# Optimization experiments

Hardware: AMD Instinct MI355X
Metric: run time of the kernel (lower is better)

The kernel has to match this reference:

```python
import jax, jax.numpy as jnp
import numpy as np

B_SZ, SEQ, D_MODEL, N_STATE = 4, 2048, 768, 16


def setup_inputs() -> dict:
    key = jax.random.key(0)
    ks = jax.random.split(key, 8)
    s = 1.0 / np.sqrt(D_MODEL)
    x = jax.random.normal(ks[0], (B_SZ, SEQ, D_MODEL), dtype=jnp.float32)
    W1 = jax.random.uniform(ks[1], (D_MODEL, D_MODEL), jnp.float32, -s, s)
    b1 = jax.random.uniform(ks[2], (D_MODEL,), jnp.float32, -s, s)
    W2 = jax.random.uniform(ks[3], (D_MODEL, N_STATE), jnp.float32, -s, s)
    b2 = jax.random.uniform(ks[4], (N_STATE,), jnp.float32, -s, s)
    W3 = jax.random.uniform(ks[5], (D_MODEL, N_STATE), jnp.float32, -s, s)
    b3 = jax.random.uniform(ks[6], (N_STATE,), jnp.float32, -s, s)
    # A: xavier_uniform over (d_model, state_size)
    a_bound = np.sqrt(6.0 / (D_MODEL + N_STATE))
    A = jax.random.uniform(ks[7], (D_MODEL, N_STATE), jnp.float32, -a_bound, a_bound)
    return {"x": x, "W1": W1, "b1": b1, "W2": W2, "b2": b2, "W3": W3, "b3": b3, "A": A}


def reference(x, W1, b1, W2, b2, W3, b3, A):
    # Input-dependent projections
    Bm = x @ W2 + b2                     # [b, l, n]
    Cm = x @ W3 + b3                     # [b, l, n]
    delta = jax.nn.softplus(x @ W1 + b1)  # [b, l, d]
    # Discretization (S6)
    dB = delta[..., None] * Bm[:, :, None, :]                 # [b, l, d, n]
    dA = jnp.exp(jnp.einsum('bld,dn->bldn', delta, A))        # [b, l, d, n]
    # Source initializes h to zeros, so the dA*h term vanishes (no recurrence).
    h0 = jnp.zeros_like(dB)
    h = dA * h0 + x[..., None] * dB                            # [b, l, d, n]
    y = jnp.einsum('bln,bldn->bld', Cm, h)                     # [b, l, d]
    return y
```

## Files before the change

### kernel.cpp

```cpp
#include <hip/hip_runtime.h>
#include <hip/hip_bf16.h>
#include <math.h>


#define M_ROWS 8192
#define DM 768
#define NS 16

typedef short bf16x8 __attribute__((ext_vector_type(8)));
typedef float f32x4 __attribute__((ext_vector_type(4)));

__device__ __forceinline__ unsigned short f2bf(float f) {
    union { float f; unsigned u; } v; v.f = f;
    unsigned r = v.u + 0x7FFF + ((v.u >> 16) & 1);
    return (unsigned short)(r >> 16);
}
__device__ __forceinline__ float bf2f(unsigned short h) {
    union { unsigned u; float f; } v; v.u = ((unsigned)h) << 16; return v.f;
}
__device__ __forceinline__ void async16(const void* g, void* l) {
    __builtin_amdgcn_global_load_lds(
        (const __attribute__((address_space(1))) void*)g,
        (__attribute__((address_space(3))) void*)l,
        16, 0, 0);
}
__device__ __forceinline__ float softplus_fast(float v) {
    return fmaxf(v, 0.f) + __logf(1.f + __expf(-fabsf(v)));
}

__global__ __launch_bounds__(256) void prep_kernel(
    const float* __restrict__ x,
    const float* __restrict__ W1,
    const float* __restrict__ W2,
    const float* __restrict__ W3,
    unsigned short* __restrict__ xb,
    unsigned short* __restrict__ w1t,
    unsigned short* __restrict__ w23t)
{
    __shared__ float tile[32][33];
    const int bid = blockIdx.x;
    const int tid = threadIdx.x;
    if (bid < 32) {
        const int n = bid, i = n >> 1;
        const float* src = (n & 1) ? W3 : W2;
        #pragma unroll
        for (int e = 0; e < 3; ++e) {
            int k = e * 256 + tid;
            w23t[n * DM + k] = f2bf(src[k * NS + i]);
        }
    } else if (bid < 608) {
        const int b2i = bid - 32;
        const int n0 = (b2i % 24) * 32, k0 = (b2i / 24) * 32;
        const int tx = tid & 31, ty = tid >> 5;
        #pragma unroll
        for (int i = 0; i < 4; ++i) {
            int k = ty + i * 8;
            tile[k][tx] = W1[(k0 + k) * DM + n0 + tx];
        }
        __syncthreads();
        #pragma unroll
        for (int i = 0; i < 4; ++i) {
            int n = ty + i * 8;
            w1t[(n0 + n) * DM + k0 + tx] = f2bf(tile[tx][n]);
        }
    } else {
        int i = (bid - 608) * 256 + tid;
        float4 v = ((const float4*)x)[i];
        ushort4 o;
        o.x = f2bf(v.x); o.y = f2bf(v.y); o.z = f2bf(v.z); o.w = f2bf(v.w);
        ((ushort4*)xb)[i] = o;
    }
}

__global__ __launch_bounds__(256) void gemm_fused_kernel(
    const unsigned short* __restrict__ xb,
    const unsigned short* __restrict__ w1t,
    const unsigned short* __restrict__ w23t,
    const float* __restrict__ b1,
    const float* __restrict__ b2, const float* __restrict__ b3,
    float* __restrict__ y)
{
    __shared__ unsigned short Al[128 * 64];
    __shared__ unsigned short Bl[64 * 64];
    __shared__ unsigned short Wl[32 * 64];
    __shared__ float spart[2][128];
    const int b = blockIdx.x;
    const int c = b & 7, j = b >> 3;
    const int m0 = (c * 8 + j / 12) * 128;
    const int n0 = (j % 12) * 64;
    const int tid  = threadIdx.x;
    const int lane = tid & 63;
    const int wave = tid >> 6;
    const int wm = wave >> 1, wn = wave & 1;
    const int l15 = lane & 15, quad = lane >> 4;

    f32x4 acc[4][2];
    f32x4 accP[4];
    #pragma unroll
    for (int i = 0; i < 4; ++i) {
        accP[i] = (f32x4){0.f, 0.f, 0.f, 0.f};
        #pragma unroll
        for (int jj = 0; jj < 2; ++jj)
            acc[i][jj] = (f32x4){0.f, 0.f, 0.f, 0.f};
    }

    for (int k0 = 0; k0 < DM; k0 += 64) {
        #pragma unroll
        for (int i = 0; i < 4; ++i) {
            int ch = tid + i * 256;
            int r = ch >> 3, jg = (ch & 7) ^ (r & 7);
            async16(xb + (m0 + r) * DM + k0 + jg * 8, Al + ch * 8);
        }
        #pragma unroll
        for (int i = 0; i < 2; ++i) {
            int ch = tid + i * 256;
            int r = ch >> 3, jg = (ch & 7) ^ (r & 7);
            async16(w1t + (n0 + r) * DM + k0 + jg * 8, Bl + ch * 8);
        }
        {
            int ch = tid;
            int r = ch >> 3, jg = (ch & 7) ^ (r & 7);
            async16(w23t + r * DM + k0 + jg * 8, Wl + ch * 8);
        }
        __syncthreads();

        #pragma unroll
        for (int kk = 0; kk < 2; ++kk) {
            bf16x8 bfr[2], wfr;
            #pragma unroll
            for (int jj = 0; jj < 2; ++jj) {
                int rb = wn * 32 + jj * 16 + l15;
                int jb = (kk * 4 + quad) ^ (rb & 7);
                bfr[jj] = *(const bf16x8*)(Bl + rb * 64 + jb * 8);
            }
            {
                int rw = wn * 16 + l15;
                int jw = (kk * 4 + quad) ^ (rw & 7);
                wfr = *(const bf16x8*)(Wl + rw * 64 + jw * 8);
            }
            #pragma unroll
            for (int i = 0; i < 4; ++i) {
                int rr = wm * 64 + i * 16 + l15;
                int ja = (kk * 4 + quad) ^ (rr & 7);
                bf16x8 af = *(const bf16x8*)(Al + rr * 64 + ja * 8);
                #pragma unroll
                for (int jj = 0; jj < 2; ++jj)
                    acc[i][jj] = __builtin_amdgcn_mfma_f32_16x16x32_bf16(
                        af, bfr[jj], acc[i][jj], 0, 0, 0);
                accP[i] = __builtin_amdgcn_mfma_f32_16x16x32_bf16(
                    af, wfr, accP[i], 0, 0, 0);
            }
        }
        __syncthreads();
    }

    {
        const int p = wn * 8 + (l15 >> 1);
        const float bB = b2[p], bC = b3[p];
        #pragma unroll
        for (int i = 0; i < 4; ++i) {
            float sacc[4];
            #pragma unroll
            for (int r = 0; r < 4; ++r) {
                float v = accP[i][r];
                float pv = __shfl_xor(v, 1, 64);
                sacc[r] = (l15 & 1) ? (pv + bB) * (v + bC)
                                    : (v + bB) * (pv + bC);
                sacc[r] += __shfl_xor(sacc[r], 1, 64);
                sacc[r] += __shfl_xor(sacc[r], 2, 64);
                sacc[r] += __shfl_xor(sacc[r], 4, 64);
                sacc[r] += __shfl_xor(sacc[r], 8, 64);
            }
            if (l15 == 0) {
                #pragma unroll
                for (int r = 0; r < 4; ++r)
                    spart[wn][wm * 64 + i * 16 + quad * 4 + r] = 0.5f * sacc[r];
            }
        }
    }
    __syncthreads();

    #pragma unroll
    for (int i = 0; i < 4; ++i) {
        const int rl = wm * 64 + i * 16 + quad * 4;
        const int rowbase = m0 + rl;
        float sv4[4];
        #pragma unroll
        for (int r = 0; r < 4; ++r)
            sv4[r] = spart[0][rl + r] + spart[1][rl + r];
        #pragma unroll
        for (int jj = 0; jj < 2; ++jj) {
            int gcol = n0 + wn * 32 + jj * 16 + l15;
            float bias = b1[gcol];
            #pragma unroll
            for (int r = 0; r < 4; ++r) {
                int grow = rowbase + r;
                float v = acc[i][jj][r] + bias;
                float sp = softplus_fast(v);
                float xv = bf2f(xb[grow * DM + gcol]);
                y[grow * DM + gcol] = xv * sp * sv4[r];
            }
        }
    }
}

extern "C" void kernel_launch(void* const* d_in, const int* in_sizes, int n_in,
                              void* d_out, int out_size, void* d_ws, size_t ws_size,
                              hipStream_t stream) {
    const float* x  = (const float*)d_in[0];
    const float* W1 = (const float*)d_in[1];
    const float* b1 = (const float*)d_in[2];
    const float* W2 = (const float*)d_in[3];
    const float* b2 = (const float*)d_in[4];
    const float* W3 = (const float*)d_in[5];
    const float* b3 = (const float*)d_in[6];
    float* y = (float*)d_out;

    unsigned short* xb   = (unsigned short*)d_ws;
    unsigned short* w1t  = (unsigned short*)((char*)d_ws + 12582912);
    unsigned short* w23t = (unsigned short*)((char*)d_ws + 13762560);

    prep_kernel<<<6752, 256, 0, stream>>>(x, W1, W2, W3, xb, w1t, w23t);
    gemm_fused_kernel<<<768, 256, 0, stream>>>(xb, w1t, w23t, b1, b2, b3, y);
}
```

Measured before the change: 112.1 us.

## Fuse x bf16 conversion into GEMM A-tile load, drop xb staging buffer

```diff
diff --git a/kernel.cpp b/kernel.cpp
--- a/kernel.cpp
+++ b/kernel.cpp
@@ -8,6 +8,7 @@
 #define NS 16
 
 typedef short bf16x8 __attribute__((ext_vector_type(8)));
+typedef unsigned short u16x8 __attribute__((ext_vector_type(8)));
 typedef float f32x4 __attribute__((ext_vector_type(4)));
 
 __device__ __forceinline__ unsigned short f2bf(float f) {
@@ -15,8 +16,9 @@
     unsigned r = v.u + 0x7FFF + ((v.u >> 16) & 1);
     return (unsigned short)(r >> 16);
 }
-__device__ __forceinline__ float bf2f(unsigned short h) {
-    union { unsigned u; float f; } v; v.u = ((unsigned)h) << 16; return v.f;
+__device__ __forceinline__ unsigned short cvtbf(float f) {
+    __hip_bfloat16 h = __float2bfloat16(f);
+    return *reinterpret_cast<unsigned short*>(&h);
 }
 __device__ __forceinline__ void async16(const void* g, void* l) {
     __builtin_amdgcn_global_load_lds(
@@ -29,11 +31,9 @@
 }
 
 __global__ __launch_bounds__(256) void prep_kernel(
-    const float* __restrict__ x,
     const float* __restrict__ W1,
     const float* __restrict__ W2,
     const float* __restrict__ W3,
-    unsigned short* __restrict__ xb,
     unsigned short* __restrict__ w1t,
     unsigned short* __restrict__ w23t)
 {
@@ -48,7 +48,7 @@
             int k = e * 256 + tid;
             w23t[n * DM + k] = f2bf(src[k * NS + i]);
         }
-    } else if (bid < 608) {
+    } else {
         const int b2i = bid - 32;
         const int n0 = (b2i % 24) * 32, k0 = (b2i / 24) * 32;
         const int tx = tid & 31, ty = tid >> 5;
@@ -63,17 +63,11 @@
             int n = ty + i * 8;
             w1t[(n0 + n) * DM + k0 + tx] = f2bf(tile[tx][n]);
         }
-    } else {
-        int i = (bid - 608) * 256 + tid;
-        float4 v = ((const float4*)x)[i];
-        ushort4 o;
-        o.x = f2bf(v.x); o.y = f2bf(v.y); o.z = f2bf(v.z); o.w = f2bf(v.w);
-        ((ushort4*)xb)[i] = o;
     }
 }
 
 __global__ __launch_bounds__(256) void gemm_fused_kernel(
-    const unsigned short* __restrict__ xb,
+    const float* __restrict__ x,
     const unsigned short* __restrict__ w1t,
     const unsigned short* __restrict__ w23t,
     const float* __restrict__ b1,
@@ -105,11 +99,14 @@
     }
 
     for (int k0 = 0; k0 < DM; k0 += 64) {
+        float4 va[8];
         #pragma unroll
         for (int i = 0; i < 4; ++i) {
             int ch = tid + i * 256;
             int r = ch >> 3, jg = (ch & 7) ^ (r & 7);
-            async16(xb + (m0 + r) * DM + k0 + jg * 8, Al + ch * 8);
+            const float4* src = (const float4*)(x + (m0 + r) * DM + k0 + jg * 8);
+            va[2 * i]     = src[0];
+            va[2 * i + 1] = src[1];
         }
         #pragma unroll
         for (int i = 0; i < 2; ++i) {
@@ -121,6 +118,17 @@
             int ch = tid;
             int r = ch >> 3, jg = (ch & 7) ^ (r & 7);
             async16(w23t + r * DM + k0 + jg * 8, Wl + ch * 8);
+        }
+        #pragma unroll
+        for (int i = 0; i < 4; ++i) {
+            int ch = tid + i * 256;
+            float4 a = va[2 * i], bb = va[2 * i + 1];
+            u16x8 o;
+            o[0] = cvtbf(a.x);  o[1] = cvtbf(a.y);
+            o[2] = cvtbf(a.z);  o[3] = cvtbf(a.w);
+            o[4] = cvtbf(bb.x); o[5] = cvtbf(bb.y);
+            o[6] = cvtbf(bb.z); o[7] = cvtbf(bb.w);
+            *(u16x8*)(Al + ch * 8) = o;
         }
         __syncthreads();
 
@@ -197,7 +205,7 @@
                 int grow = rowbase + r;
                 float v = acc[i][jj][r] + bias;
                 float sp = softplus_fast(v);
-                float xv = bf2f(xb[grow * DM + gcol]);
+                float xv = x[grow * DM + gcol];
                 y[grow * DM + gcol] = xv * sp * sv4[r];
             }
         }
@@ -216,10 +224,9 @@
     const float* b3 = (const float*)d_in[6];
     float* y = (float*)d_out;
 
-    unsigned short* xb   = (unsigned short*)d_ws;
-    unsigned short* w1t  = (unsigned short*)((char*)d_ws + 12582912);
-    unsigned short* w23t = (unsigned short*)((char*)d_ws + 13762560);
-
-    prep_kernel<<<6752, 256, 0, stream>>>(x, W1, W2, W3, xb, w1t, w23t);
-    gemm_fused_kernel<<<768, 256, 0, stream>>>(xb, w1t, w23t, b1, b2, b3, y);
-}
+    unsigned short* w1t  = (unsigned short*)d_ws;
+    unsigned short* w23t = (unsigned short*)((char*)d_ws + 1179648);
+
+    prep_kernel<<<608, 256, 0, stream>>>(W1, W2, W3, w1t, w23t);
+    gemm_fused_kernel<<<768, 256, 0, stream>>>(x, w1t, w23t, b1, b2, b3, y);
+}
```

After: 115.7 us. 3.3% more time.

## Double-buffer GEMM LDS tiles and load W2/W3 fragments directly to registers

Applied to the files above, without the earlier changes.

```diff
diff --git a/kernel.cpp b/kernel.cpp
--- a/kernel.cpp
+++ b/kernel.cpp
@@ -6,6 +6,7 @@
 #define M_ROWS 8192
 #define DM 768
 #define NS 16
+#define NT 12
 
 typedef short bf16x8 __attribute__((ext_vector_type(8)));
 typedef float f32x4 __attribute__((ext_vector_type(4)));
@@ -27,6 +28,8 @@
 __device__ __forceinline__ float softplus_fast(float v) {
     return fmaxf(v, 0.f) + __logf(1.f + __expf(-fabsf(v)));
 }
+
+#define FENCE() __builtin_amdgcn_sched_barrier(0)
 
 __global__ __launch_bounds__(256) void prep_kernel(
     const float* __restrict__ x,
@@ -80,9 +83,8 @@
     const float* __restrict__ b2, const float* __restrict__ b3,
     float* __restrict__ y)
 {
-    __shared__ unsigned short Al[128 * 64];
-    __shared__ unsigned short Bl[64 * 64];
-    __shared__ unsigned short Wl[32 * 64];
+    __shared__ unsigned short Al[2][128 * 64];
+    __shared__ unsigned short Bl[2][64 * 64];
     __shared__ float spart[2][128];
     const int b = blockIdx.x;
     const int c = b & 7, j = b >> 3;
@@ -104,45 +106,62 @@
             acc[i][jj] = (f32x4){0.f, 0.f, 0.f, 0.f};
     }
 
-    for (int k0 = 0; k0 < DM; k0 += 64) {
-        #pragma unroll
-        for (int i = 0; i < 4; ++i) {
-            int ch = tid + i * 256;
-            int r = ch >> 3, jg = (ch & 7) ^ (r & 7);
-            async16(xb + (m0 + r) * DM + k0 + jg * 8, Al + ch * 8);
-        }
-        #pragma unroll
-        for (int i = 0; i < 2; ++i) {
-            int ch = tid + i * 256;
-            int r = ch >> 3, jg = (ch & 7) ^ (r & 7);
-            async16(w1t + (n0 + r) * DM + k0 + jg * 8, Bl + ch * 8);
-        }
-        {
-            int ch = tid;
-            int r = ch >> 3, jg = (ch & 7) ^ (r & 7);
-            async16(w23t + r * DM + k0 + jg * 8, Wl + ch * 8);
-        }
-        __syncthreads();
-
+    bf16x8 vw[2][2];
+
+#define STAGE_AB(P, T) do {                                                \
+        const int k0_ = (T) * 64;                                          \
+        _Pragma("unroll")                                                  \
+        for (int i_ = 0; i_ < 4; ++i_) {               \
+            int ch_ = tid + i_ * 256;                                      \
+            int r_ = ch_ >> 3, jg_ = (ch_ & 7) ^ (r_ & 7);                 \
+            async16(xb + (m0 + r_) * DM + k0_ + jg_ * 8, &Al[P][ch_ * 8]); \
+        }                                                                  \
+        _Pragma("unroll")                                                  \
+        for (int i_ = 0; i_ < 2; ++i_) {                \
+            int ch_ = tid + i_ * 256;                                      \
+            int r_ = ch_ >> 3, jg_ = (ch_ & 7) ^ (r_ & 7);                 \
+            async16(w1t + (n0 + r_) * DM + k0_ + jg_ * 8, &Bl[P][ch_ * 8]); \
+        }                                                                  \
+    } while (0)
+
+#define LOAD_W(P, T) do {                                                  \
+        const int k0_ = (T) * 64;                                          \
+        const int rw_ = wn * 16 + l15;                                     \
+        _Pragma("unroll")                                                  \
+        for (int kk_ = 0; kk_ < 2; ++kk_)                                  \
+            vw[P][kk_] = *(const bf16x8*)(w23t + rw_ * DM + k0_ + (kk_ * 4 + quad) * 8); \
+    } while (0)
+
+    STAGE_AB(0, 0);
+    LOAD_W(0, 0);
+    FENCE();
+    asm volatile("s_waitcnt vmcnt(0) lgkmcnt(0)" ::: "memory");
+    __builtin_amdgcn_s_barrier();
+    FENCE();
+
+    #pragma unroll
+    for (int t = 0; t < NT; ++t) {
+        const int cur = t & 1;
+        if (t + 1 < NT) {
+            STAGE_AB(cur ^ 1, t + 1);
+            LOAD_W(cur ^ 1, t + 1);
+        }
+        FENCE();
         #pragma unroll
         for (int kk = 0; kk < 2; ++kk) {
-            bf16x8 bfr[2], wfr;
+            bf16x8 bfr[2];
             #pragma unroll
             for (int jj = 0; jj < 2; ++jj) {
                 int rb = wn * 32 + jj * 16 + l15;
                 int jb = (kk * 4 + quad) ^ (rb & 7);
-                bfr[jj] = *(const bf16x8*)(Bl + rb * 64 + jb * 8);
-            }
-            {
-                int rw = wn * 16 + l15;
-                int jw = (kk * 4 + quad) ^ (rw & 7);
-                wfr = *(const bf16x8*)(Wl + rw * 64 + jw * 8);
-            }
+                bfr[jj] = *(const bf16x8*)(&Bl[cur][rb * 64 + jb * 8]);
+            }
+            bf16x8 wfr = vw[cur][kk];
             #pragma unroll
             for (int i = 0; i < 4; ++i) {
                 int rr = wm * 64 + i * 16 + l15;
                 int ja = (kk * 4 + quad) ^ (rr & 7);
-                bf16x8 af = *(const bf16x8*)(Al + rr * 64 + ja * 8);
+                bf16x8 af = *(const bf16x8*)(&Al[cur][rr * 64 + ja * 8]);
                 #pragma unroll
                 for (int jj = 0; jj < 2; ++jj)
                     acc[i][jj] = __builtin_amdgcn_mfma_f32_16x16x32_bf16(
@@ -151,7 +170,10 @@
                     af, wfr, accP[i], 0, 0, 0);
             }
         }
-        __syncthreads();
+        FENCE();
+        asm volatile("s_waitcnt vmcnt(0) lgkmcnt(0)" ::: "memory");
+        __builtin_amdgcn_s_barrier();
+        FENCE();
     }
 
     {
@@ -202,6 +224,8 @@
             }
         }
     }
+#undef STAGE_AB
+#undef LOAD_W
 }
 
 extern "C" void kernel_launch(void* const* d_in, const int* in_sizes, int n_in,
```

After: 115.6 us. 3.2% more time.
